# Performance work log

Measured on AMD Instinct MI355X. Metric: run time of the kernel, lower is better.

Reference implementation:

```python
import jax, jax.numpy as jnp
import numpy as np

LN_EPS = 1e-5  # standard LayerNorm eps
OPM_EPS = 1e-3  # module's eps for the mean denominator


def layer_norm(x, g, b):
    mu = jnp.mean(x, axis=-1, keepdims=True)
    var = jnp.mean((x - mu) ** 2, axis=-1, keepdims=True)
    return (x - mu) * jax.lax.rsqrt(var + LN_EPS) * g + b


def setup_inputs() -> dict:
    key = jax.random.key(0)
    ks = jax.random.split(key, 6)
    N, L1, K, L2 = 1, 256, 128, 1024
    c_s, c_m, c_z, ch = 384, 256, 128, 32
    return {
        "s": jax.random.normal(ks[0], (N, L1, c_s), jnp.float32),
        "m": jax.random.normal(ks[1], (N, K, L2, c_m), jnp.float32),
        "ln_ab_g": jnp.ones((c_s,), jnp.float32),
        "ln_ab_b": jnp.zeros((c_s,), jnp.float32),
        "ln_ag_g": jnp.ones((c_m,), jnp.float32),
        "ln_ag_b": jnp.zeros((c_m,), jnp.float32),
        "W_ab": jax.random.normal(ks[2], (c_s, ch), jnp.float32) * 0.02,
        "b_ab": jnp.zeros((ch,), jnp.float32),
        "W_ag": jax.random.normal(ks[3], (c_m, ch), jnp.float32) * 0.02,
        "b_ag": jnp.zeros((ch,), jnp.float32),
        "W_out": jax.random.normal(ks[4], (ch * ch, c_z), jnp.float32) * 0.02,
        "b_out": jnp.zeros((c_z,), jnp.float32),
    }


def reference(s, m, ln_ab_g, ln_ab_b, ln_ag_g, ln_ag_b,
              W_ab, b_ab, W_ag, b_ag, W_out, b_out):
    # s: [N, L1, c_s], m: [N, K, L2, c_m]
    K = m.shape[1]
    ch = W_ab.shape[-1]
    c_z = W_out.shape[-1]

    a = layer_norm(s, ln_ab_g, ln_ab_b) @ W_ab + b_ab          # [N, L1, ch]
    mm = layer_norm(m, ln_ag_g, ln_ag_b) @ W_ag + b_ag          # [N, K, L2, ch]

    # In the original, `a` is repeated along K before the einsum, so it is
    # K-invariant and sum_k a[i,c] * m[k,j,e] == a[i,c] * (sum_k m[k,j,e]).
    m_sum = jnp.sum(mm, axis=1)                                  # [N, L2, ch]

    # outer[n,i,j,c,e] -> flatten (c,e) with c outer -> linear_out
    Wo = W_out.reshape(ch, ch, c_z)                              # [c, e, z]
    z = jnp.einsum('nic,nje,cez->nijz', a, m_sum, Wo) + b_out    # [N, L1, L2, c_z]

    # norm = sum over K of ones == K, plus eps
    return z / (jnp.float32(K) + OPM_EPS)
```

## Files before the change

### kernel.cpp

```cpp
#include <hip/hip_runtime.h>

#define L1V 256
#define L2V 1024
#define KV  128
#define CSV 384
#define CMV 256
#define CHV 32
#define CZV 128

typedef float f4v __attribute__((ext_vector_type(4)));
typedef float f2v __attribute__((ext_vector_type(2)));

__device__ __forceinline__ float4 f4zero() { return make_float4(0.f,0.f,0.f,0.f); }

__device__ __forceinline__ float4 nt_load4(const float4* p) {
  f4v t = __builtin_nontemporal_load((const f4v*)p);
  return make_float4(t.x, t.y, t.z, t.w);
}

__device__ __forceinline__ void ln_accum(const float4 x, float4& xs) {
  float s1 = x.x + x.y + x.z + x.w;
  float s2 = fmaf(x.x, x.x, fmaf(x.y, x.y, fmaf(x.z, x.z, x.w * x.w)));
  #pragma unroll
  for (int off = 32; off > 0; off >>= 1) {
    s1 += __shfl_xor(s1, off, 64);
    s2 += __shfl_xor(s2, off, 64);
  }
  const float mu   = s1 * (1.0f / CMV);
  const float rstd = rsqrtf(s2 * (1.0f / CMV) - mu * mu + 1e-5f);
  xs.x = fmaf(x.x - mu, rstd, xs.x);
  xs.y = fmaf(x.y - mu, rstd, xs.y);
  xs.z = fmaf(x.z - mu, rstd, xs.z);
  xs.w = fmaf(x.w - mu, rstd, xs.w);
}

__global__ __launch_bounds__(256) void msum_kernel(
    const float* __restrict__ m, const float* __restrict__ g,
    const float* __restrict__ b, const float* __restrict__ Wag,
    const float* __restrict__ bag, float* __restrict__ msum)
{
  const int j    = blockIdx.x;
  const int tid  = threadIdx.x;
  const int wave = tid >> 6;
  const int lane = tid & 63;

  const float4* base = (const float4*)m;

  float4 xs = f4zero();
  float4 x0 = nt_load4(&base[(((size_t)wave << 10) + j) * 64 + lane]);
  float4 x1 = nt_load4(&base[(((size_t)(wave + 4) << 10) + j) * 64 + lane]);

  for (int k = wave; k < KV; k += 8) {
    float4 n0 = f4zero(), n1 = f4zero();
    if (k + 8  < KV) n0 = nt_load4(&base[(((size_t)(k + 8)  << 10) + j) * 64 + lane]);
    if (k + 12 < KV) n1 = nt_load4(&base[(((size_t)(k + 12) << 10) + j) * 64 + lane]);
    ln_accum(x0, xs);
    ln_accum(x1, xs);
    x0 = n0; x1 = n1;
  }

  __shared__ float xsum[4][CMV];
  ((float4*)xsum[wave])[lane] = xs;
  __syncthreads();

  __shared__ float y[CMV];
  y[tid] = (xsum[0][tid] + xsum[1][tid] + xsum[2][tid] + xsum[3][tid]) * g[tid]
           + (float)KV * b[tid];
  __syncthreads();

  const int c     = tid & 31;
  const int chunk = tid >> 5;
  float p = 0.f;
  #pragma unroll
  for (int q = 0; q < 32; ++q) {
    const int e = (chunk << 5) + q;
    p = fmaf(y[e], Wag[(e << 5) + c], p);
  }
  __shared__ float pr[256];
  pr[tid] = p;
  __syncthreads();
  if (tid < 32) {
    float acc = 0.f;
    #pragma unroll
    for (int r = 0; r < 8; ++r) acc += pr[tid + (r << 5)];
    msum[(j << 5) + tid] = acc + (float)KV * bag[tid];
  }
}

__global__ __launch_bounds__(384) void a_kernel(
    const float* __restrict__ s, const float* __restrict__ g,
    const float* __restrict__ b, const float* __restrict__ Wab,
    const float* __restrict__ bab, float* __restrict__ a)
{
  const int i    = blockIdx.x;
  const int tid  = threadIdx.x;
  const int wave = tid >> 6;
  const int lane = tid & 63;

  const float x = s[i * CSV + tid];
  float s1 = x, s2 = x * x;
  #pragma unroll
  for (int off = 32; off > 0; off >>= 1) {
    s1 += __shfl_xor(s1, off, 64);
    s2 += __shfl_xor(s2, off, 64);
  }
  __shared__ float r1[6], r2[6];
  if (lane == 0) { r1[wave] = s1; r2[wave] = s2; }
  __syncthreads();
  float t1 = 0.f, t2 = 0.f;
  #pragma unroll
  for (int w = 0; w < 6; ++w) { t1 += r1[w]; t2 += r2[w]; }
  const float mu   = t1 * (1.0f / CSV);
  const float rstd = rsqrtf(t2 * (1.0f / CSV) - mu * mu + 1e-5f);

  __shared__ float y[CSV];
  y[tid] = (x - mu) * rstd * g[tid] + b[tid];
  __syncthreads();

  const int c     = tid & 31;
  const int chunk = tid >> 5;
  float p = 0.f;
  #pragma unroll
  for (int q = 0; q < 32; ++q) {
    const int e = (chunk << 5) + q;
    p = fmaf(y[e], Wab[(e << 5) + c], p);
  }
  __shared__ float pr[CSV];
  pr[tid] = p;
  __syncthreads();
  if (tid < 32) {
    float acc = 0.f;
    #pragma unroll
    for (int r = 0; r < 12; ++r) acc += pr[tid + (r << 5)];
    a[(i << 5) + tid] = acc + bab[tid];
  }
}

__global__ __launch_bounds__(256) void t_kernel(
    const float* __restrict__ a, const float* __restrict__ Wout,
    float* __restrict__ T)
{
  const int tid = threadIdx.x;
  const int idx = (blockIdx.x << 8) + tid;
  const int i0  = blockIdx.y << 4;

  __shared__ float as[16 * 32];
  #pragma unroll
  for (int r = 0; r < 2; ++r) {
    const int t = (r << 8) + tid;
    as[t] = a[(i0 << 5) + t];
  }
  __syncthreads();

  float w[32];
  #pragma unroll
  for (int c = 0; c < 32; ++c) w[c] = Wout[(c << 12) + idx];

  #pragma unroll 4
  for (int ii = 0; ii < 16; ++ii) {
    float acc = 0.f;
    #pragma unroll
    for (int c = 0; c < 32; ++c)
      acc = fmaf(as[(ii << 5) + c], w[c], acc);
    T[((size_t)(i0 + ii) << 12) + idx] = acc;
  }
}

__global__ __launch_bounds__(256) void out_kernel(
    const float* __restrict__ msum, const float* __restrict__ T,
    const float* __restrict__ bout, float* __restrict__ out)
{
  const int half = blockIdx.x;
  const int i    = blockIdx.y;
  const int wid  = __builtin_amdgcn_readfirstlane((int)(threadIdx.x >> 6));
  const int lane = threadIdx.x & 63;
  const int z0   = lane << 1;

  const float inv_norm = 1.0f / ((float)KV + 1e-3f);

  float2 Tr[32];
  #pragma unroll
  for (int e = 0; e < 32; ++e) {
    const float2 t = *(const float2*)(T + ((size_t)i << 12) + (e << 7) + z0);
    Tr[e] = make_float2(t.x * inv_norm, t.y * inv_norm);
  }
  float2 bz = *(const float2*)(bout + z0);
  bz.x *= inv_norm; bz.y *= inv_norm;

  const int j0 = (half << 9) + (wid << 7);
  float* const outp = out + ((size_t)i << 17);

  float4 mA[8], mB[8];

#define LOADROW(BUF, J) do {                                                \
    const float4* mr = (const float4*)(msum + ((size_t)(J) << 5));          \
    _Pragma("unroll")                                                       \
    for (int q = 0; q < 8; ++q) BUF[q] = mr[q];                             \
  } while (0)

#define FMA_STORE(BUF, J) do {                                              \
    float ax = bz.x, ay = bz.y;                                             \
    _Pragma("unroll")                                                       \
    for (int q = 0; q < 8; ++q) {                                           \
      const float4 mq = BUF[q];                                             \
      ax = fmaf(mq.x, Tr[(q<<2)+0].x, ax); ay = fmaf(mq.x, Tr[(q<<2)+0].y, ay); \
      ax = fmaf(mq.y, Tr[(q<<2)+1].x, ax); ay = fmaf(mq.y, Tr[(q<<2)+1].y, ay); \
      ax = fmaf(mq.z, Tr[(q<<2)+2].x, ax); ay = fmaf(mq.z, Tr[(q<<2)+2].y, ay); \
      ax = fmaf(mq.w, Tr[(q<<2)+3].x, ax); ay = fmaf(mq.w, Tr[(q<<2)+3].y, ay); \
    }                                                                       \
    f2v ov; ov.x = ax; ov.y = ay;                                           \
    __builtin_nontemporal_store(ov,                                         \
        (f2v*)(outp + ((size_t)(J) << 7) + z0));                            \
  } while (0)

  LOADROW(mA, j0);
  for (int jj = 0; jj < 128; jj += 2) {
    LOADROW(mB, j0 + jj + 1);
    FMA_STORE(mA, j0 + jj);
    if (jj + 2 < 128) LOADROW(mA, j0 + jj + 2);
    FMA_STORE(mB, j0 + jj + 1);
  }
#undef LOADROW
#undef FMA_STORE
}

extern "C" void kernel_launch(void* const* d_in, const int* in_sizes, int n_in,
                              void* d_out, int out_size, void* d_ws, size_t ws_size,
                              hipStream_t stream) {
  (void)in_sizes; (void)n_in; (void)out_size; (void)ws_size;
  const float* s    = (const float*)d_in[0];
  const float* m    = (const float*)d_in[1];
  const float* g_ab = (const float*)d_in[2];
  const float* b_ab = (const float*)d_in[3];
  const float* g_ag = (const float*)d_in[4];
  const float* b_ag = (const float*)d_in[5];
  const float* Wab  = (const float*)d_in[6];
  const float* bab  = (const float*)d_in[7];
  const float* Wag  = (const float*)d_in[8];
  const float* bag  = (const float*)d_in[9];
  const float* Wout = (const float*)d_in[10];
  const float* bout = (const float*)d_in[11];
  float* out = (float*)d_out;

  float* msum = (float*)d_ws;
  float* a    = msum + 32768;
  float* T    = a + 8192;

  hipLaunchKernelGGL(msum_kernel, dim3(1024), dim3(256), 0, stream,
                     m, g_ag, b_ag, Wag, bag, msum);
  hipLaunchKernelGGL(a_kernel, dim3(256), dim3(384), 0, stream,
                     s, g_ab, b_ab, Wab, bab, a);
  hipLaunchKernelGGL(t_kernel, dim3(16, 16), dim3(256), 0, stream,
                     a, Wout, T);
  hipLaunchKernelGGL(out_kernel, dim3(2, 256), dim3(256), 0, stream,
                     msum, T, bout, out);
}
```

Before: 269.8 us.

## Fuse msum, a and T kernels into one launch; split out_kernel across more blocks

Merges the m-reduction kernel, the s LayerNorm+projection kernel and the T (a·W_out) kernel into a single launch. The first 1024 blocks compute msum and the extra 256 blocks each recompute a for 16 rows and then produce T. This removes two kernel launches and lets the small a/T work overlap with the bandwidth-bound m reduction. The price is redundant recomputation of a across the 16 column blocks. out_kernel now uses 4 blocks per row instead of 2, each wave covering 64 j values, which raises parallelism but makes each block reload the T registers for half as much output.

```diff
diff --git a/kernel.cpp b/kernel.cpp
--- a/kernel.cpp
+++ b/kernel.cpp
@@ -34,135 +34,121 @@
   xs.w = fmaf(x.w - mu, rstd, xs.w);
 }
 
-__global__ __launch_bounds__(256) void msum_kernel(
-    const float* __restrict__ m, const float* __restrict__ g,
-    const float* __restrict__ b, const float* __restrict__ Wag,
-    const float* __restrict__ bag, float* __restrict__ msum)
+__global__ __launch_bounds__(256) void front_kernel(
+    const float* __restrict__ m,  const float* __restrict__ gm,
+    const float* __restrict__ bm, const float* __restrict__ Wg,
+    const float* __restrict__ bg, float* __restrict__ msum,
+    const float* __restrict__ s,  const float* __restrict__ gs,
+    const float* __restrict__ bs, const float* __restrict__ Wa,
+    const float* __restrict__ ba, const float* __restrict__ Wout,
+    float* __restrict__ T)
 {
-  const int j    = blockIdx.x;
   const int tid  = threadIdx.x;
   const int wave = tid >> 6;
   const int lane = tid & 63;
 
-  const float4* base = (const float4*)m;
-
-  float4 xs = f4zero();
-  float4 x0 = nt_load4(&base[(((size_t)wave << 10) + j) * 64 + lane]);
-  float4 x1 = nt_load4(&base[(((size_t)(wave + 4) << 10) + j) * 64 + lane]);
-
-  for (int k = wave; k < KV; k += 8) {
-    float4 n0 = f4zero(), n1 = f4zero();
-    if (k + 8  < KV) n0 = nt_load4(&base[(((size_t)(k + 8)  << 10) + j) * 64 + lane]);
-    if (k + 12 < KV) n1 = nt_load4(&base[(((size_t)(k + 12) << 10) + j) * 64 + lane]);
-    ln_accum(x0, xs);
-    ln_accum(x1, xs);
-    x0 = n0; x1 = n1;
-  }
-
-  __shared__ float xsum[4][CMV];
-  ((float4*)xsum[wave])[lane] = xs;
-  __syncthreads();
-
-  __shared__ float y[CMV];
-  y[tid] = (xsum[0][tid] + xsum[1][tid] + xsum[2][tid] + xsum[3][tid]) * g[tid]
-           + (float)KV * b[tid];
-  __syncthreads();
-
-  const int c     = tid & 31;
-  const int chunk = tid >> 5;
-  float p = 0.f;
-  #pragma unroll
-  for (int q = 0; q < 32; ++q) {
-    const int e = (chunk << 5) + q;
-    p = fmaf(y[e], Wag[(e << 5) + c], p);
-  }
-  __shared__ float pr[256];
-  pr[tid] = p;
-  __syncthreads();
-  if (tid < 32) {
-    float acc = 0.f;
+  if (blockIdx.x < 1024) {
+    const int j = blockIdx.x;
+    const float4* base = (const float4*)m;
+
+    float4 xs = f4zero();
+    float4 x0 = nt_load4(&base[(((size_t)wave << 10) + j) * 64 + lane]);
+    float4 x1 = nt_load4(&base[(((size_t)(wave + 4) << 10) + j) * 64 + lane]);
+
+    for (int k = wave; k < KV; k += 8) {
+      float4 n0 = f4zero(), n1 = f4zero();
+      if (k + 8  < KV) n0 = nt_load4(&base[(((size_t)(k + 8)  << 10) + j) * 64 + lane]);
+      if (k + 12 < KV) n1 = nt_load4(&base[(((size_t)(k + 12) << 10) + j) * 64 + lane]);
+      ln_accum(x0, xs);
+      ln_accum(x1, xs);
+      x0 = n0; x1 = n1;
+    }
+
+    __shared__ float xsum[4][CMV];
+    ((float4*)xsum[wave])[lane] = xs;
+    __syncthreads();
+
+    __shared__ float y[CMV];
+    y[tid] = (xsum[0][tid] + xsum[1][tid] + xsum[2][tid] + xsum[3][tid]) * gm[tid]
+             + (float)KV * bm[tid];
+    __syncthreads();
+
+    const int c     = tid & 31;
+    const int chunk = tid >> 5;
+    float p = 0.f;
     #pragma unroll
-    for (int r = 0; r < 8; ++r) acc += pr[tid + (r << 5)];
-    msum[(j << 5) + tid] = acc + (float)KV * bag[tid];
-  }
-}
-
-__global__ __launch_bounds__(384) void a_kernel(
-    const float* __restrict__ s, const float* __restrict__ g,
-    const float* __restrict__ b, const float* __restrict__ Wab,
-    const float* __restrict__ bab, float* __restrict__ a)
-{
-  const int i    = blockIdx.x;
-  const int tid  = threadIdx.x;
-  const int wave = tid >> 6;
-  const int lane = tid & 63;
-
-  const float x = s[i * CSV + tid];
-  float s1 = x, s2 = x * x;
-  #pragma unroll
-  for (int off = 32; off > 0; off >>= 1) {
-    s1 += __shfl_xor(s1, off, 64);
-    s2 += __shfl_xor(s2, off, 64);
-  }
-  __shared__ float r1[6], r2[6];
-  if (lane == 0) { r1[wave] = s1; r2[wave] = s2; }
-  __syncthreads();
-  float t1 = 0.f, t2 = 0.f;
-  #pragma unroll
-  for (int w = 0; w < 6; ++w) { t1 += r1[w]; t2 += r2[w]; }
-  const float mu   = t1 * (1.0f / CSV);
-  const float rstd = rsqrtf(t2 * (1.0f / CSV) - mu * mu + 1e-5f);
-
-  __shared__ float y[CSV];
-  y[tid] = (x - mu) * rstd * g[tid] + b[tid];
-  __syncthreads();
-
-  const int c     = tid & 31;
-  const int chunk = tid >> 5;
-  float p = 0.f;
-  #pragma unroll
-  for (int q = 0; q < 32; ++q) {
-    const int e = (chunk << 5) + q;
-    p = fmaf(y[e], Wab[(e << 5) + c], p);
-  }
-  __shared__ float pr[CSV];
-  pr[tid] = p;
-  __syncthreads();
-  if (tid < 32) {
-    float acc = 0.f;
+    for (int q = 0; q < 32; ++q) {
+      const int e = (chunk << 5) + q;
+      p = fmaf(y[e], Wg[(e << 5) + c], p);
+    }
+    __shared__ float pr[256];
+    pr[tid] = p;
+    __syncthreads();
+    if (tid < 32) {
+      float acc = 0.f;
+      #pragma unroll
+      for (int r = 0; r < 8; ++r) acc += pr[tid + (r << 5)];
+      msum[(j << 5) + tid] = acc + (float)KV * bg[tid];
+    }
+  } else {
+    const int b   = blockIdx.x - 1024;
+    const int bx  = b & 15;
+    const int i0  = (b >> 4) << 4;
+    const int idx = (bx << 8) + tid;
+
+    __shared__ float ylds[8][CSV];
+    __shared__ float as_[16 * CHV];
+
     #pragma unroll
-    for (int r = 0; r < 12; ++r) acc += pr[tid + (r << 5)];
-    a[(i << 5) + tid] = acc + bab[tid];
-  }
-}
-
-__global__ __launch_bounds__(256) void t_kernel(
-    const float* __restrict__ a, const float* __restrict__ Wout,
-    float* __restrict__ T)
-{
-  const int tid = threadIdx.x;
-  const int idx = (blockIdx.x << 8) + tid;
-  const int i0  = blockIdx.y << 4;
-
-  __shared__ float as[16 * 32];
-  #pragma unroll
-  for (int r = 0; r < 2; ++r) {
-    const int t = (r << 8) + tid;
-    as[t] = a[(i0 << 5) + t];
-  }
-  __syncthreads();
-
-  float w[32];
-  #pragma unroll
-  for (int c = 0; c < 32; ++c) w[c] = Wout[(c << 12) + idx];
-
-  #pragma unroll 4
-  for (int ii = 0; ii < 16; ++ii) {
-    float acc = 0.f;
+    for (int halfp = 0; halfp < 2; ++halfp) {
+      #pragma unroll
+      for (int rr = 0; rr < 2; ++rr) {
+        const int r = (wave << 1) + rr;
+        const int i = i0 + (halfp << 3) + r;
+        float xv[6];
+        #pragma unroll
+        for (int q = 0; q < 6; ++q) xv[q] = s[i * CSV + (q << 6) + lane];
+        float s1 = 0.f, s2 = 0.f;
+        #pragma unroll
+        for (int q = 0; q < 6; ++q) { s1 += xv[q]; s2 = fmaf(xv[q], xv[q], s2); }
+        #pragma unroll
+        for (int off = 32; off > 0; off >>= 1) {
+          s1 += __shfl_xor(s1, off, 64);
+          s2 += __shfl_xor(s2, off, 64);
+        }
+        const float mu   = s1 * (1.0f / CSV);
+        const float rstd = rsqrtf(s2 * (1.0f / CSV) - mu * mu + 1e-5f);
+        #pragma unroll
+        for (int q = 0; q < 6; ++q) {
+          const int e = (q << 6) + lane;
+          ylds[r][e] = (xv[q] - mu) * rstd * gs[e] + bs[e];
+        }
+      }
+      __syncthreads();
+      {
+        const int ii = tid >> 5;
+        const int c  = tid & 31;
+        float acc = ba[c];
+        #pragma unroll 8
+        for (int e = 0; e < CSV; ++e)
+          acc = fmaf(ylds[ii][e], Wa[(e << 5) + c], acc);
+        as_[(((halfp << 3) + ii) << 5) + c] = acc;
+      }
+      __syncthreads();
+    }
+
+    float w[32];
     #pragma unroll
-    for (int c = 0; c < 32; ++c)
-      acc = fmaf(as[(ii << 5) + c], w[c], acc);
-    T[((size_t)(i0 + ii) << 12) + idx] = acc;
+    for (int c = 0; c < 32; ++c) w[c] = Wout[(c << 12) + idx];
+
+    #pragma unroll 4
+    for (int ii = 0; ii < 16; ++ii) {
+      float acc = 0.f;
+      #pragma unroll
+      for (int c = 0; c < 32; ++c)
+        acc = fmaf(as_[(ii << 5) + c], w[c], acc);
+      T[((size_t)(i0 + ii) << 12) + idx] = acc;
+    }
   }
 }
 
@@ -170,11 +156,11 @@
     const float* __restrict__ msum, const float* __restrict__ T,
     const float* __restrict__ bout, float* __restrict__ out)
 {
-  const int half = blockIdx.x;
-  const int i    = blockIdx.y;
-  const int wid  = __builtin_amdgcn_readfirstlane((int)(threadIdx.x >> 6));
-  const int lane = threadIdx.x & 63;
-  const int z0   = lane << 1;
+  const int quart = blockIdx.x;
+  const int i     = blockIdx.y;
+  const int wid   = __builtin_amdgcn_readfirstlane((int)(threadIdx.x >> 6));
+  const int lane  = threadIdx.x & 63;
+  const int z0    = lane << 1;
 
   const float inv_norm = 1.0f / ((float)KV + 1e-3f);
 
@@ -187,7 +173,7 @@
   float2 bz = *(const float2*)(bout + z0);
   bz.x *= inv_norm; bz.y *= inv_norm;
 
-  const int j0 = (half << 9) + (wid << 7);
+  const int j0 = (quart << 8) + (wid << 6);
   float* const outp = out + ((size_t)i << 17);
 
   float4 mA[8], mB[8];
@@ -214,10 +200,10 @@
   } while (0)
 
   LOADROW(mA, j0);
-  for (int jj = 0; jj < 128; jj += 2) {
+  for (int jj = 0; jj < 64; jj += 2) {
     LOADROW(mB, j0 + jj + 1);
     FMA_STORE(mA, j0 + jj);
-    if (jj + 2 < 128) LOADROW(mA, j0 + jj + 2);
+    if (jj + 2 < 64) LOADROW(mA, j0 + jj + 2);
     FMA_STORE(mB, j0 + jj + 1);
   }
 #undef LOADROW
@@ -243,15 +229,11 @@
   float* out = (float*)d_out;
 
   float* msum = (float*)d_ws;
-  float* a    = msum + 32768;
-  float* T    = a + 8192;
-
-  hipLaunchKernelGGL(msum_kernel, dim3(1024), dim3(256), 0, stream,
-                     m, g_ag, b_ag, Wag, bag, msum);
-  hipLaunchKernelGGL(a_kernel, dim3(256), dim3(384), 0, stream,
-                     s, g_ab, b_ab, Wab, bab, a);
-  hipLaunchKernelGGL(t_kernel, dim3(16, 16), dim3(256), 0, stream,
-                     a, Wout, T);
-  hipLaunchKernelGGL(out_kernel, dim3(2, 256), dim3(256), 0, stream,
+  float* T    = msum + 32768 + 8192;
+
+  hipLaunchKernelGGL(front_kernel, dim3(1280), dim3(256), 0, stream,
+                     m, g_ag, b_ag, Wag, bag, msum,
+                     s, g_ab, b_ab, Wab, bab, Wout, T);
+  hipLaunchKernelGGL(out_kernel, dim3(4, 256), dim3(256), 0, stream,
                      msum, T, bout, out);
 }
```

Measured after the change: 279.5 us. +3.6%, slower.
